# Optimization experiments

Measured on AMD Instinct MI355X. Metric: run time of the kernel, lower is better.

Reference implementation:

```python
import jax, jax.numpy as jnp
import numpy as np
from jax import lax

B, N, C, H = 8, 1024, 384, 6
D = C // H
SCALE = D ** -0.5
EPS = 1e-5


def setup_inputs() -> dict:
    key = jax.random.key(0)
    ks = jax.random.split(key, 10)
    s = 0.02
    return {
        "x": jax.random.normal(ks[0], (B, N, C), jnp.float32),
        "w_qkv": jax.random.normal(ks[1], (3 * C, C), jnp.float32) * s,
        "w_proj": jax.random.normal(ks[2], (C, C), jnp.float32) * s,
        "b_proj": jax.random.normal(ks[3], (C,), jnp.float32) * s,
        "w_kq": jax.random.normal(ks[4], (H, 1, 3, 3), jnp.float32) * 0.1,   # depthwise (groups=H)
        "b_kq": jax.random.normal(ks[5], (H,), jnp.float32) * 0.1,
        "w_head": jax.random.normal(ks[6], (H, H, 1, 1), jnp.float32) * 0.1,  # 1x1 head-mixing conv
        "b_head": jax.random.normal(ks[7], (H,), jnp.float32) * 0.1,
        "gn_w": jnp.ones((H,), jnp.float32),
        "gn_b": jnp.zeros((H,), jnp.float32),
    }


def reference(x, w_qkv, w_proj, b_proj, w_kq, b_kq, w_head, b_head, gn_w, gn_b):
    # qkv projection (torch Linear: y = x @ W.T)
    qkv = (x @ w_qkv.T).reshape(B, N, 3, H, D).transpose(2, 0, 3, 1, 4)  # [3,B,H,N,D]
    q, k, v = qkv[0], qkv[1], qkv[2]

    # attention logits [B,H,N,N]
    logits = jnp.einsum("bhnd,bhmd->bhnm", q, k) * SCALE

    # depthwise (groups=H) 3x3 conv over the NxN logit map
    logits = lax.conv_general_dilated(
        logits, w_kq, window_strides=(1, 1), padding=((1, 1), (1, 1)),
        dimension_numbers=("NCHW", "OIHW", "NCHW"), feature_group_count=H,
    ) + b_kq[None, :, None, None]

    attn = jax.nn.softmax(logits, axis=-1)

    # 1x1 conv mixing heads
    attn = jnp.einsum("oh,bhnm->bonm", w_head[:, :, 0, 0], attn) + b_head[None, :, None, None]

    # GroupNorm(num_groups=H, channels=H): per (b, head) stats over NxN
    mean = attn.mean(axis=(2, 3), keepdims=True)
    var = ((attn - mean) ** 2).mean(axis=(2, 3), keepdims=True)
    attn = (attn - mean) * lax.rsqrt(var + EPS)
    attn = attn * gn_w[None, :, None, None] + gn_b[None, :, None, None]

    out = jnp.einsum("bhnm,bhmd->bhnd", attn, v)
    out = out.transpose(0, 2, 1, 3).reshape(B, N, C)
    return out @ w_proj.T + b_proj
```

## Files before the change

### kernel.cpp

```cpp
#include <hip/hip_runtime.h>

typedef unsigned short u16;
typedef __attribute__((ext_vector_type(8))) short short8;
typedef __attribute__((ext_vector_type(4))) float f32x4;

#define MFMA(a, b, c) __builtin_amdgcn_mfma_f32_16x16x32_bf16((a), (b), (c), 0, 0, 0)

__device__ inline float bf2f(u16 u) {
  union { unsigned int i; float f; } w; w.i = ((unsigned int)u) << 16; return w.f;
}
__device__ inline u16 f2bf(float x) {
  union { float f; unsigned int i; } u; u.f = x;
  unsigned int r = u.i + 0x7fffu + ((u.i >> 16) & 1u);
  return (u16)(r >> 16);
}
__device__ inline unsigned int pk2(float a, float b) {
  return (unsigned int)f2bf(a) | ((unsigned int)f2bf(b) << 16);
}
__device__ inline void unpack8(uint4 v, float* f) {
  union { unsigned int i; float g; } c;
  c.i = v.x << 16;          f[0] = c.g;
  c.i = v.x & 0xffff0000u;  f[1] = c.g;
  c.i = v.y << 16;          f[2] = c.g;
  c.i = v.y & 0xffff0000u;  f[3] = c.g;
  c.i = v.z << 16;          f[4] = c.g;
  c.i = v.z & 0xffff0000u;  f[5] = c.g;
  c.i = v.w << 16;          f[6] = c.g;
  c.i = v.w & 0xffff0000u;  f[7] = c.g;
}

static const size_t SZ_QKV = (size_t)48 * 1024 * 64 * 2;
static const size_t SZ_MAP = (size_t)48 * 1024 * 1024 * 2;
static const size_t OFF_Q  = 0;
static const size_t OFF_K  = OFF_Q + SZ_QKV;
static const size_t OFF_VT = OFF_K + SZ_QKV;
static const size_t OFF_S  = OFF_VT + SZ_QKV;
static const size_t OFF_UG = OFF_S;
static const size_t OFF_QM = OFF_S + SZ_MAP;
static const size_t OFF_OT = OFF_QM + SZ_MAP;
static const size_t OFF_ST = OFF_OT + SZ_QKV;
static const size_t OFF_CS = OFF_ST + 896;
static const size_t OFF_AD = OFF_CS + 12288;
static const size_t OFF_AL = OFF_AD + 12288;

__global__ __launch_bounds__(256) void k_qkv(const float* __restrict__ x,
                                             const float* __restrict__ w,
                                             u16* __restrict__ qb,
                                             u16* __restrict__ kb,
                                             u16* __restrict__ vT) {
  __shared__ u16 As[128 * 64];
  __shared__ u16 Bs[128 * 64];
  const int t = threadIdx.x;
  const int m0 = blockIdx.x * 128;
  const int n0 = blockIdx.y * 128;
  const int wave = t >> 6, lane = t & 63;
  const int wm = (wave & 1) * 64, wn = (wave >> 1) * 64;
  const int fr = lane & 15;
  const int fk = (lane >> 4) * 8;
  f32x4 acc[4][4] = {};
  for (int k0 = 0; k0 < 384; k0 += 64) {
#pragma unroll
    for (int i = 0; i < 4; ++i) {
      int e = (i * 256 + t) * 8;
      int row = e >> 6, col = e & 63;
      const float* xp = &x[(size_t)(m0 + row) * 384 + k0 + col];
      const float* wp = &w[(size_t)(n0 + row) * 384 + k0 + col];
      float4 a0 = *(const float4*)xp, a1 = *(const float4*)(xp + 4);
      uint4 av; av.x = pk2(a0.x, a0.y); av.y = pk2(a0.z, a0.w);
      av.z = pk2(a1.x, a1.y); av.w = pk2(a1.z, a1.w);
      *(uint4*)&As[e] = av;
      float4 b0 = *(const float4*)wp, b1 = *(const float4*)(wp + 4);
      uint4 bv; bv.x = pk2(b0.x, b0.y); bv.y = pk2(b0.z, b0.w);
      bv.z = pk2(b1.x, b1.y); bv.w = pk2(b1.z, b1.w);
      *(uint4*)&Bs[e] = bv;
    }
    __syncthreads();
#pragma unroll
    for (int ks = 0; ks < 2; ++ks) {
      const int ko = ks * 32 + fk;
      short8 a[4], b[4];
#pragma unroll
      for (int mi = 0; mi < 4; ++mi) a[mi] = *(const short8*)&As[(wm + mi * 16 + fr) * 64 + ko];
#pragma unroll
      for (int ni = 0; ni < 4; ++ni) b[ni] = *(const short8*)&Bs[(wn + ni * 16 + fr) * 64 + ko];
#pragma unroll
      for (int mi = 0; mi < 4; ++mi)
#pragma unroll
        for (int ni = 0; ni < 4; ++ni) acc[mi][ni] = MFMA(a[mi], b[ni], acc[mi][ni]);
    }
    __syncthreads();
  }
#pragma unroll
  for (int mi = 0; mi < 4; ++mi) {
#pragma unroll
    for (int ni = 0; ni < 4; ++ni) {
      int gc = n0 + wn + ni * 16 + fr;
      int s = gc / 384;
      int rem = gc - s * 384;
      int h = rem >> 6, d = rem & 63;
#pragma unroll
      for (int r = 0; r < 4; ++r) {
        int gm = m0 + wm + mi * 16 + (lane >> 4) * 4 + r;
        int b_ = gm >> 10, n = gm & 1023;
        u16 val = f2bf(acc[mi][ni][r]);
        size_t base = (size_t)(b_ * 6 + h) << 16;
        if (s == 0)      qb[base + (size_t)n * 64 + d] = val;
        else if (s == 1) kb[base + (size_t)n * 64 + d] = val;
        else             vT[base + (size_t)d * 1024 + n] = val;
      }
    }
  }
}

__global__ __launch_bounds__(256) void k_qk(const u16* __restrict__ qb,
                                            const u16* __restrict__ kb,
                                            u16* __restrict__ S) {
  __shared__ u16 As[128 * 64];
  __shared__ u16 Bs[128 * 64];
  const int t = threadIdx.x;
  const int m0 = blockIdx.x * 128, n0 = blockIdx.y * 128;
  const int bh = blockIdx.z;
  const u16* A = qb + ((size_t)bh << 16);
  const u16* Bp = kb + ((size_t)bh << 16);
  const int wave = t >> 6, lane = t & 63;
  const int wm = (wave & 1) * 64, wn = (wave >> 1) * 64;
  const int fr = lane & 15;
  const int fk = (lane >> 4) * 8;
  f32x4 acc[4][4] = {};
#pragma unroll
  for (int i = 0; i < 4; ++i) {
    int e = (i * 256 + t) * 8;
    *(uint4*)&As[e] = *(const uint4*)&A[(size_t)m0 * 64 + e];
    *(uint4*)&Bs[e] = *(const uint4*)&Bp[(size_t)n0 * 64 + e];
  }
  __syncthreads();
#pragma unroll
  for (int ks = 0; ks < 2; ++ks) {
    const int ko = ks * 32 + fk;
    short8 a[4], b[4];
#pragma unroll
    for (int mi = 0; mi < 4; ++mi) a[mi] = *(const short8*)&As[(wm + mi * 16 + fr) * 64 + ko];
#pragma unroll
    for (int ni = 0; ni < 4; ++ni) b[ni] = *(const short8*)&Bs[(wn + ni * 16 + fr) * 64 + ko];
#pragma unroll
    for (int mi = 0; mi < 4; ++mi)
#pragma unroll
      for (int ni = 0; ni < 4; ++ni) acc[mi][ni] = MFMA(a[mi], b[ni], acc[mi][ni]);
  }
  const size_t sb = (size_t)bh << 20;
#pragma unroll
  for (int mi = 0; mi < 4; ++mi)
#pragma unroll
    for (int ni = 0; ni < 4; ++ni) {
      int gc = n0 + wn + ni * 16 + fr;
#pragma unroll
      for (int r = 0; r < 4; ++r) {
        int gm = m0 + wm + mi * 16 + (lane >> 4) * 4 + r;
        S[sb + (size_t)gm * 1024 + gc] = f2bf(acc[mi][ni][r] * 0.125f);
      }
    }
}

__global__ __launch_bounds__(256) void k_conv_softmax(const u16* __restrict__ S,
                                                      const float* __restrict__ w_kq,
                                                      u16* __restrict__ Qb) {
  __shared__ u16 Sr[10 * 1040];
  __shared__ float red[4];
  const int t = threadIdx.x;
  const int bh = blockIdx.y;
  const int h = bh % 6;
  const int r0 = blockIdx.x * 8;
  const u16* Sp = S + ((size_t)bh << 20);
  float wv[9];
#pragma unroll
  for (int i = 0; i < 9; ++i) wv[i] = w_kq[h * 9 + i];
  if (t < 10) { Sr[t * 1040 + 7] = 0; Sr[t * 1040 + 1032] = 0; }
#pragma unroll
  for (int c = 0; c < 5; ++c) {
    int e = (c * 256 + t) * 8;
    int i = e >> 10, col = e & 1023;
    int g = r0 - 1 + i;
    uint4 val = make_uint4(0u, 0u, 0u, 0u);
    if (g >= 0 && g < 1024) val = *(const uint4*)&Sp[(size_t)g * 1024 + col];
    *(uint4*)&Sr[i * 1040 + 8 + col] = val;
  }
  __syncthreads();
  const int half = t >> 7;
  const int lane = t & 63;
  const int m0 = (t & 127) * 8;
  for (int pass = 0; pass < 4; ++pass) {
    int rr = pass * 2 + half;
    float o8[8];
#pragma unroll
    for (int j = 0; j < 8; ++j) o8[j] = 0.f;
#pragma unroll
    for (int i = 0; i < 3; ++i) {
      const u16* rowp = &Sr[(rr + i) * 1040 + 8];
      float left = bf2f(rowp[m0 - 1]);
      float md[8];
      unpack8(*(const uint4*)&rowp[m0], md);
      float right = bf2f(rowp[m0 + 8]);
      float w0 = wv[i * 3 + 0], w1 = wv[i * 3 + 1], w2 = wv[i * 3 + 2];
      o8[0] += w0 * left + w1 * md[0] + w2 * md[1];
#pragma unroll
      for (int j = 1; j < 7; ++j) o8[j] += w0 * md[j - 1] + w1 * md[j] + w2 * md[j + 1];
      o8[7] += w0 * md[6] + w1 * md[7] + w2 * right;
    }
    float mx = o8[0];
#pragma unroll
    for (int j = 1; j < 8; ++j) mx = fmaxf(mx, o8[j]);
    for (int off = 32; off; off >>= 1) mx = fmaxf(mx, __shfl_xor(mx, off, 64));
    if (lane == 0) red[t >> 6] = mx;
    __syncthreads();
    float rmax = fmaxf(red[half * 2], red[half * 2 + 1]);
    __syncthreads();
    float e8[8], s = 0.f;
#pragma unroll
    for (int j = 0; j < 8; ++j) { e8[j] = __expf(o8[j] - rmax); s += e8[j]; }
    for (int off = 32; off; off >>= 1) s += __shfl_xor(s, off, 64);
    if (lane == 0) red[t >> 6] = s;
    __syncthreads();
    float rsum = red[half * 2] + red[half * 2 + 1];
    __syncthreads();
    float scale = 1024.f / rsum;
    unsigned int pk[4];
#pragma unroll
    for (int jj = 0; jj < 4; ++jj)
      pk[jj] = pk2(e8[2 * jj] * scale - 1.f, e8[2 * jj + 1] * scale - 1.f);
    int n = r0 + rr;
    *(uint4*)&Qb[((size_t)bh << 20) + (size_t)n * 1024 + m0] = make_uint4(pk[0], pk[1], pk[2], pk[3]);
  }
}

__global__ __launch_bounds__(256) void k_colsum(const u16* __restrict__ vT,
                                                float* __restrict__ colsum) {
  __shared__ float acc[64];
  const int t = threadIdx.x;
  const int bh = blockIdx.x;
  if (t < 64) acc[t] = 0.f;
  __syncthreads();
  const int lane = t & 63;
  for (int c = 0; c < 32; ++c) {
    size_t l = (size_t)c * 2048 + (size_t)t * 8;
    uint4 u = *(const uint4*)&vT[((size_t)bh << 16) + l];
    float f[8];
    unpack8(u, f);
    float part = f[0] + f[1] + f[2] + f[3] + f[4] + f[5] + f[6] + f[7];
    for (int off = 32; off; off >>= 1) part += __shfl_xor(part, off, 64);
    if (lane == 0) atomicAdd(&acc[(int)(l >> 10)], part);
  }
  __syncthreads();
  if (t < 64) colsum[bh * 64 + t] = acc[t];
}

__global__ __launch_bounds__(256) void k_pvmix(const u16* __restrict__ Qm,
                                               const u16* __restrict__ vT,
                                               const float* __restrict__ wh,
                                               float* __restrict__ Ug,
                                               float* __restrict__ stats) {
  __shared__ u16 Am[64 * 72];
  __shared__ u16 Vm[64 * 72];
  const int t = threadIdx.x;
  const int n0 = blockIdx.x * 64;
  const int bo = blockIdx.y;
  const int b_ = bo / 6, o = bo - b_ * 6;
  const int wave = t >> 6, lane = t & 63;
  const int fr = lane & 15, quad = lane >> 4;
  const int srow = t >> 3, smg8 = (t & 7) * 8;
  float wo[6];
#pragma unroll
  for (int hh = 0; hh < 6; ++hh) wo[hh] = wh[o * 6 + hh];
  const size_t qbase = ((size_t)(b_ * 6)) << 20;
  const u16* vp = vT + ((size_t)bo << 16);
  uint4 qpre[2][6];
  uint4 vpre[2];
  {
    const int m = smg8;
#pragma unroll
    for (int i = 0; i < 2; ++i)
#pragma unroll
      for (int hh = 0; hh < 6; ++hh)
        qpre[i][hh] = *(const uint4*)&Qm[qbase + (((size_t)hh) << 20) +
                                         (size_t)(n0 + i * 32 + srow) * 1024 + m];
    vpre[0] = *(const uint4*)&vp[(size_t)srow * 1024 + m];
    vpre[1] = *(const uint4*)&vp[(size_t)(32 + srow) * 1024 + m];
  }
  f32x4 acc[4] = {};
  float s1 = 0.f, s2 = 0.f;
  for (int mc = 0; mc < 16; ++mc) {
    __syncthreads();
#pragma unroll
    for (int i = 0; i < 2; ++i) {
      float mix[8] = {0.f, 0.f, 0.f, 0.f, 0.f, 0.f, 0.f, 0.f};
#pragma unroll
      for (int hh = 0; hh < 6; ++hh) {
        float qf[8];
        unpack8(qpre[i][hh], qf);
        float w = wo[hh];
#pragma unroll
        for (int j = 0; j < 8; ++j) mix[j] += w * qf[j];
      }
#pragma unroll
      for (int j = 0; j < 8; ++j) { s1 += mix[j]; s2 += mix[j] * mix[j]; }
      uint4 pk4;
      pk4.x = pk2(mix[0], mix[1]); pk4.y = pk2(mix[2], mix[3]);
      pk4.z = pk2(mix[4], mix[5]); pk4.w = pk2(mix[6], mix[7]);
      *(uint4*)&Am[(i * 32 + srow) * 72 + smg8] = pk4;
    }
    *(uint4*)&Vm[srow * 72 + smg8] = vpre[0];
    *(uint4*)&Vm[(32 + srow) * 72 + smg8] = vpre[1];
    if (mc < 15) {
      const int m = (mc + 1) * 64 + smg8;
#pragma unroll
      for (int i = 0; i < 2; ++i)
#pragma unroll
        for (int hh = 0; hh < 6; ++hh)
          qpre[i][hh] = *(const uint4*)&Qm[qbase + (((size_t)hh) << 20) +
                                           (size_t)(n0 + i * 32 + srow) * 1024 + m];
      vpre[0] = *(const uint4*)&vp[(size_t)srow * 1024 + m];
      vpre[1] = *(const uint4*)&vp[(size_t)(32 + srow) * 1024 + m];
    }
    __syncthreads();
#pragma unroll
    for (int ks = 0; ks < 2; ++ks) {
      short8 a = *(const short8*)&Am[(wave * 16 + fr) * 72 + ks * 32 + quad * 8];
#pragma unroll
      for (int ni = 0; ni < 4; ++ni) {
        short8 b = *(const short8*)&Vm[(ni * 16 + fr) * 72 + ks * 32 + quad * 8];
        acc[ni] = MFMA(a, b, acc[ni]);
      }
    }
  }
#pragma unroll
  for (int ni = 0; ni < 4; ++ni) {
    int d = ni * 16 + fr;
#pragma unroll
    for (int r = 0; r < 4; ++r) {
      int n = n0 + wave * 16 + quad * 4 + r;
      Ug[((size_t)(bo * 1024 + n)) * 64 + d] = acc[ni][r];
    }
  }
  for (int off = 32; off; off >>= 1) {
    s1 += __shfl_xor(s1, off, 64);
    s2 += __shfl_xor(s2, off, 64);
  }
  if (lane == 0) {
    atomicAdd(&stats[bo * 2 + 0], s1);
    atomicAdd(&stats[bo * 2 + 1], s2);
  }
}

__global__ __launch_bounds__(256) void k_finalize(const float* __restrict__ stats,
                                                  const float* __restrict__ colsum,
                                                  const float* __restrict__ gn_w,
                                                  const float* __restrict__ gn_b,
                                                  float* __restrict__ addend,
                                                  float* __restrict__ alphaArr) {
  int gid = blockIdx.x * 256 + threadIdx.x;
  int bo = gid >> 6, d = gid & 63;
  int o = bo % 6;
  float s1 = stats[bo * 2], s2 = stats[bo * 2 + 1];
  const float inv = 1.f / 1048576.f;
  float mu = s1 * inv;
  float var = s2 * inv - mu * mu;
  float alpha = gn_w[o] * rsqrtf(var + 1e-5f * 1048576.f);
  float beta = gn_b[o] - alpha * mu;
  addend[gid] = beta * colsum[gid];
  if (d == 0) alphaArr[bo] = alpha;
}

__global__ __launch_bounds__(256) void k_apply(const float* __restrict__ Ug,
                                               const float* __restrict__ alphaArr,
                                               const float* __restrict__ addend,
                                               u16* __restrict__ otmp) {
  int i = blockIdx.x * 256 + threadIdx.x;
  int e = i * 4;
  int d4 = e & 63;
  int n = (e >> 6) & 1023;
  int bo = e >> 16;
  float al = alphaArr[bo];
  const float* ap = &addend[bo * 64 + d4];
  float4 u = *(const float4*)&Ug[e];
  int b = bo / 6, o = bo - b * 6;
  uint2 w;
  w.x = pk2(al * u.x + ap[0], al * u.y + ap[1]);
  w.y = pk2(al * u.z + ap[2], al * u.w + ap[3]);
  *(uint2*)&otmp[((size_t)(b * 1024 + n)) * 384 + o * 64 + d4] = w;
}

__global__ __launch_bounds__(256) void k_proj(const u16* __restrict__ A,
                                              const float* __restrict__ w,
                                              const float* __restrict__ bias,
                                              float* __restrict__ out) {
  __shared__ u16 As[128 * 64];
  __shared__ u16 Bs[128 * 64];
  const int t = threadIdx.x;
  const int m0 = blockIdx.x * 128;
  const int n0 = blockIdx.y * 128;
  const int wave = t >> 6, lane = t & 63;
  const int wm = (wave & 1) * 64, wn = (wave >> 1) * 64;
  const int fr = lane & 15;
  const int fk = (lane >> 4) * 8;
  f32x4 acc[4][4] = {};
  for (int k0 = 0; k0 < 384; k0 += 64) {
#pragma unroll
    for (int i = 0; i < 4; ++i) {
      int e = (i * 256 + t) * 8;
      int row = e >> 6, col = e & 63;
      *(uint4*)&As[e] = *(const uint4*)&A[(size_t)(m0 + row) * 384 + k0 + col];
      const float* wp = &w[(size_t)(n0 + row) * 384 + k0 + col];
      float4 b0 = *(const float4*)wp, b1 = *(const float4*)(wp + 4);
      uint4 bv; bv.x = pk2(b0.x, b0.y); bv.y = pk2(b0.z, b0.w);
      bv.z = pk2(b1.x, b1.y); bv.w = pk2(b1.z, b1.w);
      *(uint4*)&Bs[e] = bv;
    }
    __syncthreads();
#pragma unroll
    for (int ks = 0; ks < 2; ++ks) {
      const int ko = ks * 32 + fk;
      short8 a[4], b[4];
#pragma unroll
      for (int mi = 0; mi < 4; ++mi) a[mi] = *(const short8*)&As[(wm + mi * 16 + fr) * 64 + ko];
#pragma unroll
      for (int ni = 0; ni < 4; ++ni) b[ni] = *(const short8*)&Bs[(wn + ni * 16 + fr) * 64 + ko];
#pragma unroll
      for (int mi = 0; mi < 4; ++mi)
#pragma unroll
        for (int ni = 0; ni < 4; ++ni) acc[mi][ni] = MFMA(a[mi], b[ni], acc[mi][ni]);
    }
    __syncthreads();
  }
#pragma unroll
  for (int mi = 0; mi < 4; ++mi)
#pragma unroll
    for (int ni = 0; ni < 4; ++ni) {
      int gc = n0 + wn + ni * 16 + fr;
      float bv = bias[gc];
#pragma unroll
      for (int r = 0; r < 4; ++r) {
        int gm = m0 + wm + mi * 16 + (lane >> 4) * 4 + r;
        out[(size_t)gm * 384 + gc] = acc[mi][ni][r] + bv;
      }
    }
}

extern "C" void kernel_launch(void* const* d_in, const int* in_sizes, int n_in,
                              void* d_out, int out_size, void* d_ws, size_t ws_size,
                              hipStream_t stream) {
  (void)in_sizes; (void)n_in; (void)out_size; (void)ws_size;
  const float* x      = (const float*)d_in[0];
  const float* w_qkv  = (const float*)d_in[1];
  const float* w_proj = (const float*)d_in[2];
  const float* b_proj = (const float*)d_in[3];
  const float* w_kq   = (const float*)d_in[4];
  const float* w_head = (const float*)d_in[6];
  const float* gn_w   = (const float*)d_in[8];
  const float* gn_b   = (const float*)d_in[9];

  char* ws = (char*)d_ws;
  u16*   qb      = (u16*)(ws + OFF_Q);
  u16*   kb      = (u16*)(ws + OFF_K);
  u16*   vT      = (u16*)(ws + OFF_VT);
  u16*   Sb      = (u16*)(ws + OFF_S);
  float* Ug      = (float*)(ws + OFF_UG);
  u16*   Qm      = (u16*)(ws + OFF_QM);
  u16*   otmp    = (u16*)(ws + OFF_OT);
  float* stats   = (float*)(ws + OFF_ST);
  float* colsum  = (float*)(ws + OFF_CS);
  float* addend  = (float*)(ws + OFF_AD);
  float* alphaA  = (float*)(ws + OFF_AL);

  hipMemsetAsync(stats, 0, 512, stream);
  k_qkv<<<dim3(64, 9), 256, 0, stream>>>(x, w_qkv, qb, kb, vT);
  k_qk<<<dim3(8, 8, 48), 256, 0, stream>>>(qb, kb, Sb);
  k_conv_softmax<<<dim3(128, 48), 256, 0, stream>>>(Sb, w_kq, Qm);
  k_colsum<<<dim3(48), 256, 0, stream>>>(vT, colsum);
  k_pvmix<<<dim3(16, 48), 256, 0, stream>>>(Qm, vT, w_head, Ug, stats);
  k_finalize<<<dim3(12), 256, 0, stream>>>(stats, colsum, gn_w, gn_b, addend, alphaA);
  k_apply<<<dim3(3072), 256, 0, stream>>>(Ug, alphaA, addend, otmp);
  k_proj<<<dim3(64, 3), 256, 0, stream>>>(otmp, w_proj, b_proj, (float*)d_out);
}
```

Before: 307.2 us.

## Fuse head-mixing into conv-softmax and split PV over key halves

```diff
diff --git a/kernel.cpp b/kernel.cpp
--- a/kernel.cpp
+++ b/kernel.cpp
@@ -43,6 +43,8 @@
 static const size_t OFF_AD = OFF_CS + 12288;
 static const size_t OFF_AL = OFF_AD + 12288;
 
+static const size_t U_ELEMS = (size_t)48 * 1024 * 64;
+
 __global__ __launch_bounds__(256) void k_qkv(const float* __restrict__ x,
                                              const float* __restrict__ w,
                                              u16* __restrict__ qb,
@@ -161,41 +163,47 @@
     }
 }
 
-__global__ __launch_bounds__(256) void k_conv_softmax(const u16* __restrict__ S,
-                                                      const float* __restrict__ w_kq,
-                                                      u16* __restrict__ Qb) {
-  __shared__ u16 Sr[10 * 1040];
-  __shared__ float red[4];
-  const int t = threadIdx.x;
-  const int bh = blockIdx.y;
-  const int h = bh % 6;
-  const int r0 = blockIdx.x * 8;
-  const u16* Sp = S + ((size_t)bh << 20);
-  float wv[9];
-#pragma unroll
-  for (int i = 0; i < 9; ++i) wv[i] = w_kq[h * 9 + i];
-  if (t < 10) { Sr[t * 1040 + 7] = 0; Sr[t * 1040 + 1032] = 0; }
-#pragma unroll
-  for (int c = 0; c < 5; ++c) {
-    int e = (c * 256 + t) * 8;
-    int i = e >> 10, col = e & 1023;
-    int g = r0 - 1 + i;
+__global__ __launch_bounds__(256) void k_conv_softmax_mix(const u16* __restrict__ S,
+                                                          const float* __restrict__ w_kq,
+                                                          const float* __restrict__ wh,
+                                                          u16* __restrict__ Qb) {
+  __shared__ u16 Sr[24 * 1040];
+  __shared__ float redA[4], redB[4];
+  const int t = threadIdx.x;
+  const int b = blockIdx.y;
+  const int n0 = blockIdx.x * 2;
+  if (t < 24) { Sr[t * 1040 + 7] = 0; Sr[t * 1040 + 1032] = 0; }
+#pragma unroll
+  for (int c = 0; c < 12; ++c) {
+    int lid = c * 256 + t;
+    int hrow = lid >> 7;
+    int col8 = (lid & 127) * 8;
+    int h = hrow >> 2, i = hrow & 3;
+    int g = n0 - 1 + i;
     uint4 val = make_uint4(0u, 0u, 0u, 0u);
-    if (g >= 0 && g < 1024) val = *(const uint4*)&Sp[(size_t)g * 1024 + col];
-    *(uint4*)&Sr[i * 1040 + 8 + col] = val;
+    if (g >= 0 && g < 1024)
+      val = *(const uint4*)&S[(((size_t)(b * 6 + h)) << 20) + (size_t)g * 1024 + col8];
+    *(uint4*)&Sr[hrow * 1040 + 8 + col8] = val;
   }
   __syncthreads();
-  const int half = t >> 7;
+  const int row = t >> 7;
+  const int wave = t >> 6;
   const int lane = t & 63;
   const int m0 = (t & 127) * 8;
-  for (int pass = 0; pass < 4; ++pass) {
-    int rr = pass * 2 + half;
-    float o8[8];
-#pragma unroll
-    for (int j = 0; j < 8; ++j) o8[j] = 0.f;
+  const int n = n0 + row;
+  float mix[6][8];
+#pragma unroll
+  for (int o = 0; o < 6; ++o)
+#pragma unroll
+    for (int j = 0; j < 8; ++j) mix[o][j] = 0.f;
+  for (int h = 0; h < 6; ++h) {
+    float wv[9];
+#pragma unroll
+    for (int i = 0; i < 9; ++i) wv[i] = w_kq[h * 9 + i];
+    float o8[8] = {0.f, 0.f, 0.f, 0.f, 0.f, 0.f, 0.f, 0.f};
 #pragma unroll
     for (int i = 0; i < 3; ++i) {
-      const u16* rowp = &Sr[(rr + i) * 1040 + 8];
+      const u16* rowp = &Sr[(h * 4 + row + i) * 1040 + 8];
       float left = bf2f(rowp[m0 - 1]);
       float md[8];
       unpack8(*(const uint4*)&rowp[m0], md);
@@ -210,25 +218,34 @@
 #pragma unroll
     for (int j = 1; j < 8; ++j) mx = fmaxf(mx, o8[j]);
     for (int off = 32; off; off >>= 1) mx = fmaxf(mx, __shfl_xor(mx, off, 64));
-    if (lane == 0) red[t >> 6] = mx;
-    __syncthreads();
-    float rmax = fmaxf(red[half * 2], red[half * 2 + 1]);
-    __syncthreads();
+    if (lane == 0) redA[wave] = mx;
+    __syncthreads();
+    float rmax = fmaxf(redA[row * 2], redA[row * 2 + 1]);
     float e8[8], s = 0.f;
 #pragma unroll
     for (int j = 0; j < 8; ++j) { e8[j] = __expf(o8[j] - rmax); s += e8[j]; }
     for (int off = 32; off; off >>= 1) s += __shfl_xor(s, off, 64);
-    if (lane == 0) red[t >> 6] = s;
-    __syncthreads();
-    float rsum = red[half * 2] + red[half * 2 + 1];
-    __syncthreads();
+    if (lane == 0) redB[wave] = s;
+    __syncthreads();
+    float rsum = redB[row * 2] + redB[row * 2 + 1];
     float scale = 1024.f / rsum;
-    unsigned int pk[4];
-#pragma unroll
-    for (int jj = 0; jj < 4; ++jj)
-      pk[jj] = pk2(e8[2 * jj] * scale - 1.f, e8[2 * jj + 1] * scale - 1.f);
-    int n = r0 + rr;
-    *(uint4*)&Qb[((size_t)bh << 20) + (size_t)n * 1024 + m0] = make_uint4(pk[0], pk[1], pk[2], pk[3]);
+    const float w0h = wh[0 * 6 + h], w1h = wh[1 * 6 + h], w2h = wh[2 * 6 + h],
+                w3h = wh[3 * 6 + h], w4h = wh[4 * 6 + h], w5h = wh[5 * 6 + h];
+#pragma unroll
+    for (int j = 0; j < 8; ++j) {
+      float p = e8[j] * scale - 1.f;
+      mix[0][j] += w0h * p; mix[1][j] += w1h * p; mix[2][j] += w2h * p;
+      mix[3][j] += w3h * p; mix[4][j] += w4h * p; mix[5][j] += w5h * p;
+    }
+  }
+#pragma unroll
+  for (int o = 0; o < 6; ++o) {
+    uint4 pk4;
+    pk4.x = pk2(mix[o][0], mix[o][1]);
+    pk4.y = pk2(mix[o][2], mix[o][3]);
+    pk4.z = pk2(mix[o][4], mix[o][5]);
+    pk4.w = pk2(mix[o][6], mix[o][7]);
+    *(uint4*)&Qb[(((size_t)(b * 6 + o)) << 20) + (size_t)n * 1024 + m0] = pk4;
   }
 }
 
@@ -253,70 +270,51 @@
   if (t < 64) colsum[bh * 64 + t] = acc[t];
 }
 
-__global__ __launch_bounds__(256) void k_pvmix(const u16* __restrict__ Qm,
-                                               const u16* __restrict__ vT,
-                                               const float* __restrict__ wh,
-                                               float* __restrict__ Ug,
-                                               float* __restrict__ stats) {
+__global__ __launch_bounds__(256) void k_pv(const u16* __restrict__ Qm,
+                                            const u16* __restrict__ vT,
+                                            float* __restrict__ Ug,
+                                            float* __restrict__ stats) {
   __shared__ u16 Am[64 * 72];
   __shared__ u16 Vm[64 * 72];
   const int t = threadIdx.x;
   const int n0 = blockIdx.x * 64;
   const int bo = blockIdx.y;
-  const int b_ = bo / 6, o = bo - b_ * 6;
+  const int z = blockIdx.z;
   const int wave = t >> 6, lane = t & 63;
   const int fr = lane & 15, quad = lane >> 4;
   const int srow = t >> 3, smg8 = (t & 7) * 8;
-  float wo[6];
-#pragma unroll
-  for (int hh = 0; hh < 6; ++hh) wo[hh] = wh[o * 6 + hh];
-  const size_t qbase = ((size_t)(b_ * 6)) << 20;
+  const u16* qp = Qm + ((size_t)bo << 20);
   const u16* vp = vT + ((size_t)bo << 16);
-  uint4 qpre[2][6];
-  uint4 vpre[2];
+  const int mbase = z * 512;
+  uint4 qpre[2], vpre[2];
   {
-    const int m = smg8;
-#pragma unroll
-    for (int i = 0; i < 2; ++i)
-#pragma unroll
-      for (int hh = 0; hh < 6; ++hh)
-        qpre[i][hh] = *(const uint4*)&Qm[qbase + (((size_t)hh) << 20) +
-                                         (size_t)(n0 + i * 32 + srow) * 1024 + m];
+    const int m = mbase + smg8;
+    qpre[0] = *(const uint4*)&qp[(size_t)(n0 + srow) * 1024 + m];
+    qpre[1] = *(const uint4*)&qp[(size_t)(n0 + 32 + srow) * 1024 + m];
     vpre[0] = *(const uint4*)&vp[(size_t)srow * 1024 + m];
     vpre[1] = *(const uint4*)&vp[(size_t)(32 + srow) * 1024 + m];
   }
   f32x4 acc[4] = {};
   float s1 = 0.f, s2 = 0.f;
-  for (int mc = 0; mc < 16; ++mc) {
-    __syncthreads();
-#pragma unroll
-    for (int i = 0; i < 2; ++i) {
-      float mix[8] = {0.f, 0.f, 0.f, 0.f, 0.f, 0.f, 0.f, 0.f};
-#pragma unroll
-      for (int hh = 0; hh < 6; ++hh) {
-        float qf[8];
-        unpack8(qpre[i][hh], qf);
-        float w = wo[hh];
-#pragma unroll
-        for (int j = 0; j < 8; ++j) mix[j] += w * qf[j];
-      }
-#pragma unroll
-      for (int j = 0; j < 8; ++j) { s1 += mix[j]; s2 += mix[j] * mix[j]; }
-      uint4 pk4;
-      pk4.x = pk2(mix[0], mix[1]); pk4.y = pk2(mix[2], mix[3]);
-      pk4.z = pk2(mix[4], mix[5]); pk4.w = pk2(mix[6], mix[7]);
-      *(uint4*)&Am[(i * 32 + srow) * 72 + smg8] = pk4;
-    }
+  for (int mc = 0; mc < 8; ++mc) {
+    __syncthreads();
+    *(uint4*)&Am[srow * 72 + smg8] = qpre[0];
+    *(uint4*)&Am[(32 + srow) * 72 + smg8] = qpre[1];
     *(uint4*)&Vm[srow * 72 + smg8] = vpre[0];
     *(uint4*)&Vm[(32 + srow) * 72 + smg8] = vpre[1];
-    if (mc < 15) {
-      const int m = (mc + 1) * 64 + smg8;
-#pragma unroll
-      for (int i = 0; i < 2; ++i)
-#pragma unroll
-        for (int hh = 0; hh < 6; ++hh)
-          qpre[i][hh] = *(const uint4*)&Qm[qbase + (((size_t)hh) << 20) +
-                                           (size_t)(n0 + i * 32 + srow) * 1024 + m];
+    {
+      float f[8];
+      unpack8(qpre[0], f);
+#pragma unroll
+      for (int j = 0; j < 8; ++j) { s1 += f[j]; s2 += f[j] * f[j]; }
+      unpack8(qpre[1], f);
+#pragma unroll
+      for (int j = 0; j < 8; ++j) { s1 += f[j]; s2 += f[j] * f[j]; }
+    }
+    if (mc < 7) {
+      const int m = mbase + (mc + 1) * 64 + smg8;
+      qpre[0] = *(const uint4*)&qp[(size_t)(n0 + srow) * 1024 + m];
+      qpre[1] = *(const uint4*)&qp[(size_t)(n0 + 32 + srow) * 1024 + m];
       vpre[0] = *(const uint4*)&vp[(size_t)srow * 1024 + m];
       vpre[1] = *(const uint4*)&vp[(size_t)(32 + srow) * 1024 + m];
     }
@@ -331,13 +329,14 @@
       }
     }
   }
+  float* Up = Ug + (size_t)z * U_ELEMS;
 #pragma unroll
   for (int ni = 0; ni < 4; ++ni) {
     int d = ni * 16 + fr;
 #pragma unroll
     for (int r = 0; r < 4; ++r) {
       int n = n0 + wave * 16 + quad * 4 + r;
-      Ug[((size_t)(bo * 1024 + n)) * 64 + d] = acc[ni][r];
+      Up[((size_t)(bo * 1024 + n)) * 64 + d] = acc[ni][r];
     }
   }
   for (int off = 32; off; off >>= 1) {
@@ -380,11 +379,13 @@
   int bo = e >> 16;
   float al = alphaArr[bo];
   const float* ap = &addend[bo * 64 + d4];
-  float4 u = *(const float4*)&Ug[e];
+  float4 u0 = *(const float4*)&Ug[e];
+  float4 u1 = *(const float4*)&Ug[U_ELEMS + e];
+  float ux = u0.x + u1.x, uy = u0.y + u1.y, uz = u0.z + u1.z, uw = u0.w + u1.w;
   int b = bo / 6, o = bo - b * 6;
   uint2 w;
-  w.x = pk2(al * u.x + ap[0], al * u.y + ap[1]);
-  w.y = pk2(al * u.z + ap[2], al * u.w + ap[3]);
+  w.x = pk2(al * ux + ap[0], al * uy + ap[1]);
+  w.y = pk2(al * uz + ap[2], al * uw + ap[3]);
   *(uint2*)&otmp[((size_t)(b * 1024 + n)) * 384 + o * 64 + d4] = w;
 }
 
@@ -473,9 +474,9 @@
   hipMemsetAsync(stats, 0, 512, stream);
   k_qkv<<<dim3(64, 9), 256, 0, stream>>>(x, w_qkv, qb, kb, vT);
   k_qk<<<dim3(8, 8, 48), 256, 0, stream>>>(qb, kb, Sb);
-  k_conv_softmax<<<dim3(128, 48), 256, 0, stream>>>(Sb, w_kq, Qm);
+  k_conv_softmax_mix<<<dim3(512, 8), 256, 0, stream>>>(Sb, w_kq, w_head, Qm);
   k_colsum<<<dim3(48), 256, 0, stream>>>(vT, colsum);
-  k_pvmix<<<dim3(16, 48), 256, 0, stream>>>(Qm, vT, w_head, Ug, stats);
+  k_pv<<<dim3(16, 48, 2), 256, 0, stream>>>(Qm, vT, Ug, stats);
   k_finalize<<<dim3(12), 256, 0, stream>>>(stats, colsum, gn_w, gn_b, addend, alphaA);
   k_apply<<<dim3(3072), 256, 0, stream>>>(Ug, alphaA, addend, otmp);
   k_proj<<<dim3(64, 3), 256, 0, stream>>>(otmp, w_proj, b_proj, (float*)d_out);
```

After: 345.9 us. 12.6% more time.

## Stage GEMM epilogues through LDS for coalesced stores and fuse colsum into QKV

Applied to the files above, without the earlier changes.

```diff
diff --git a/kernel.cpp b/kernel.cpp
--- a/kernel.cpp
+++ b/kernel.cpp
@@ -43,13 +43,15 @@
 static const size_t OFF_AD = OFF_CS + 12288;
 static const size_t OFF_AL = OFF_AD + 12288;
 
-__global__ __launch_bounds__(256) void k_qkv(const float* __restrict__ x,
-                                             const float* __restrict__ w,
-                                             u16* __restrict__ qb,
-                                             u16* __restrict__ kb,
-                                             u16* __restrict__ vT) {
-  __shared__ u16 As[128 * 64];
-  __shared__ u16 Bs[128 * 64];
+__global__ __launch_bounds__(256, 3) void k_qkv(const float* __restrict__ x,
+                                                const float* __restrict__ w,
+                                                u16* __restrict__ qb,
+                                                u16* __restrict__ kb,
+                                                u16* __restrict__ vT,
+                                                float* __restrict__ colsum) {
+  __shared__ u16 SH[16384];
+  u16* As = SH;
+  u16* Bs = SH + 8192;
   const int t = threadIdx.x;
   const int m0 = blockIdx.x * 128;
   const int n0 = blockIdx.y * 128;
@@ -90,33 +92,58 @@
     }
     __syncthreads();
   }
-#pragma unroll
-  for (int mi = 0; mi < 4; ++mi) {
+  u16* st = &SH[wave * 4096];
+  const int gcb = n0 + wn;
+  const int s = gcb / 384;
+  const int remb = gcb - s * 384;
+  const int h = remb >> 6;
+#pragma unroll
+  for (int mi = 0; mi < 4; ++mi)
+#pragma unroll
+    for (int ni = 0; ni < 4; ++ni)
+#pragma unroll
+      for (int r = 0; r < 4; ++r) {
+        int rl = mi * 16 + (lane >> 4) * 4 + r;
+        int cl = ni * 16 + fr;
+        u16 val = f2bf(acc[mi][ni][r]);
+        if (s == 2) st[cl * 64 + rl] = val;
+        else        st[rl * 64 + cl] = val;
+      }
+  const int gm0 = m0 + wm;
+  const int b_ = gm0 >> 10;
+  const size_t base = (size_t)(b_ * 6 + h) << 16;
+  const int nloc = gm0 & 1023;
+  const int r8 = lane >> 3, c8 = (lane & 7) * 8;
+#pragma unroll
+  for (int i = 0; i < 8; ++i) {
+    int lrow = i * 8 + r8;
+    uint4 v = *(const uint4*)&st[lrow * 64 + c8];
+    if (s == 0)      *(uint4*)&qb[base + (size_t)(nloc + lrow) * 64 + c8] = v;
+    else if (s == 1) *(uint4*)&kb[base + (size_t)(nloc + lrow) * 64 + c8] = v;
+    else             *(uint4*)&vT[base + (size_t)lrow * 1024 + nloc + c8] = v;
+  }
+  if (s == 2) {
 #pragma unroll
     for (int ni = 0; ni < 4; ++ni) {
-      int gc = n0 + wn + ni * 16 + fr;
-      int s = gc / 384;
-      int rem = gc - s * 384;
-      int h = rem >> 6, d = rem & 63;
-#pragma unroll
-      for (int r = 0; r < 4; ++r) {
-        int gm = m0 + wm + mi * 16 + (lane >> 4) * 4 + r;
-        int b_ = gm >> 10, n = gm & 1023;
-        u16 val = f2bf(acc[mi][ni][r]);
-        size_t base = (size_t)(b_ * 6 + h) << 16;
-        if (s == 0)      qb[base + (size_t)n * 64 + d] = val;
-        else if (s == 1) kb[base + (size_t)n * 64 + d] = val;
-        else             vT[base + (size_t)d * 1024 + n] = val;
-      }
-    }
-  }
-}
-
-__global__ __launch_bounds__(256) void k_qk(const u16* __restrict__ qb,
-                                            const u16* __restrict__ kb,
-                                            u16* __restrict__ S) {
-  __shared__ u16 As[128 * 64];
-  __shared__ u16 Bs[128 * 64];
+      float p = 0.f;
+#pragma unroll
+      for (int mi = 0; mi < 4; ++mi)
+#pragma unroll
+        for (int r = 0; r < 4; ++r) p += bf2f(f2bf(acc[mi][ni][r]));
+      p += __shfl_xor(p, 16, 64);
+      p += __shfl_xor(p, 32, 64);
+      if ((lane >> 4) == 0)
+        atomicAdd(&colsum[(b_ * 6 + h) * 64 + ni * 16 + fr], p);
+    }
+  }
+}
+
+__global__ __launch_bounds__(256, 3) void k_qk(const u16* __restrict__ qb,
+                                               const u16* __restrict__ kb,
+                                               u16* __restrict__ S) {
+  __shared__ u16 SH[16384];
+  u16* As = SH;
+  u16* Bs = SH + 8192;
   const int t = threadIdx.x;
   const int m0 = blockIdx.x * 128, n0 = blockIdx.y * 128;
   const int bh = blockIdx.z;
@@ -147,18 +174,24 @@
 #pragma unroll
       for (int ni = 0; ni < 4; ++ni) acc[mi][ni] = MFMA(a[mi], b[ni], acc[mi][ni]);
   }
+  __syncthreads();
+  u16* st = &SH[wave * 4096];
+#pragma unroll
+  for (int mi = 0; mi < 4; ++mi)
+#pragma unroll
+    for (int ni = 0; ni < 4; ++ni)
+#pragma unroll
+      for (int r = 0; r < 4; ++r)
+        st[(mi * 16 + (lane >> 4) * 4 + r) * 64 + ni * 16 + fr] = f2bf(acc[mi][ni][r] * 0.125f);
   const size_t sb = (size_t)bh << 20;
-#pragma unroll
-  for (int mi = 0; mi < 4; ++mi)
-#pragma unroll
-    for (int ni = 0; ni < 4; ++ni) {
-      int gc = n0 + wn + ni * 16 + fr;
-#pragma unroll
-      for (int r = 0; r < 4; ++r) {
-        int gm = m0 + wm + mi * 16 + (lane >> 4) * 4 + r;
-        S[sb + (size_t)gm * 1024 + gc] = f2bf(acc[mi][ni][r] * 0.125f);
-      }
-    }
+  const int grow0 = m0 + wm, gcol0 = n0 + wn;
+  const int r8 = lane >> 3, c8 = (lane & 7) * 8;
+#pragma unroll
+  for (int i = 0; i < 8; ++i) {
+    int lrow = i * 8 + r8;
+    uint4 v = *(const uint4*)&st[lrow * 64 + c8];
+    *(uint4*)&S[sb + (size_t)(grow0 + lrow) * 1024 + gcol0 + c8] = v;
+  }
 }
 
 __global__ __launch_bounds__(256) void k_conv_softmax(const u16* __restrict__ S,
@@ -232,34 +265,14 @@
   }
 }
 
-__global__ __launch_bounds__(256) void k_colsum(const u16* __restrict__ vT,
-                                                float* __restrict__ colsum) {
-  __shared__ float acc[64];
-  const int t = threadIdx.x;
-  const int bh = blockIdx.x;
-  if (t < 64) acc[t] = 0.f;
-  __syncthreads();
-  const int lane = t & 63;
-  for (int c = 0; c < 32; ++c) {
-    size_t l = (size_t)c * 2048 + (size_t)t * 8;
-    uint4 u = *(const uint4*)&vT[((size_t)bh << 16) + l];
-    float f[8];
-    unpack8(u, f);
-    float part = f[0] + f[1] + f[2] + f[3] + f[4] + f[5] + f[6] + f[7];
-    for (int off = 32; off; off >>= 1) part += __shfl_xor(part, off, 64);
-    if (lane == 0) atomicAdd(&acc[(int)(l >> 10)], part);
-  }
-  __syncthreads();
-  if (t < 64) colsum[bh * 64 + t] = acc[t];
-}
-
 __global__ __launch_bounds__(256) void k_pvmix(const u16* __restrict__ Qm,
                                                const u16* __restrict__ vT,
                                                const float* __restrict__ wh,
                                                float* __restrict__ Ug,
                                                float* __restrict__ stats) {
-  __shared__ u16 Am[64 * 72];
-  __shared__ u16 Vm[64 * 72];
+  __shared__ u16 SH[2 * 64 * 72];
+  u16* Am = SH;
+  u16* Vm = SH + 64 * 72;
   const int t = threadIdx.x;
   const int n0 = blockIdx.x * 64;
   const int bo = blockIdx.y;
@@ -331,14 +344,19 @@
       }
     }
   }
-#pragma unroll
-  for (int ni = 0; ni < 4; ++ni) {
-    int d = ni * 16 + fr;
-#pragma unroll
-    for (int r = 0; r < 4; ++r) {
-      int n = n0 + wave * 16 + quad * 4 + r;
-      Ug[((size_t)(bo * 1024 + n)) * 64 + d] = acc[ni][r];
-    }
+  __syncthreads();
+  float* FS = (float*)SH;
+#pragma unroll
+  for (int ni = 0; ni < 4; ++ni)
+#pragma unroll
+    for (int r = 0; r < 4; ++r)
+      FS[(wave * 16 + quad * 4 + r) * 64 + ni * 16 + fr] = acc[ni][r];
+  __syncthreads();
+  float* Up = Ug + ((size_t)(bo * 1024 + n0)) * 64;
+#pragma unroll
+  for (int j = 0; j < 4; ++j) {
+    int oo = j * 1024 + t * 4;
+    *(float4*)&Up[oo] = *(const float4*)&FS[oo];
   }
   for (int off = 32; off; off >>= 1) {
     s1 += __shfl_xor(s1, off, 64);
@@ -388,12 +406,13 @@
   *(uint2*)&otmp[((size_t)(b * 1024 + n)) * 384 + o * 64 + d4] = w;
 }
 
-__global__ __launch_bounds__(256) void k_proj(const u16* __restrict__ A,
-                                              const float* __restrict__ w,
-                                              const float* __restrict__ bias,
-                                              float* __restrict__ out) {
-  __shared__ u16 As[128 * 64];
-  __shared__ u16 Bs[128 * 64];
+__global__ __launch_bounds__(256, 3) void k_proj(const u16* __restrict__ A,
+                                                 const float* __restrict__ w,
+                                                 const float* __restrict__ bias,
+                                                 float* __restrict__ out) {
+  __shared__ u16 SH[16384];
+  u16* As = SH;
+  u16* Bs = SH + 8192;
   const int t = threadIdx.x;
   const int m0 = blockIdx.x * 128;
   const int n0 = blockIdx.y * 128;
@@ -430,18 +449,32 @@
     }
     __syncthreads();
   }
-#pragma unroll
-  for (int mi = 0; mi < 4; ++mi)
-#pragma unroll
-    for (int ni = 0; ni < 4; ++ni) {
-      int gc = n0 + wn + ni * 16 + fr;
-      float bv = bias[gc];
-#pragma unroll
-      for (int r = 0; r < 4; ++r) {
-        int gm = m0 + wm + mi * 16 + (lane >> 4) * 4 + r;
-        out[(size_t)gm * 384 + gc] = acc[mi][ni][r] + bv;
+  float* FS = (float*)SH;
+  float* fst = &FS[wave * 2048];
+  float bv[4];
+#pragma unroll
+  for (int ni = 0; ni < 4; ++ni) bv[ni] = bias[n0 + wn + ni * 16 + fr];
+#pragma unroll
+  for (int half = 0; half < 2; ++half) {
+#pragma unroll
+    for (int mi2 = 0; mi2 < 2; ++mi2) {
+      int mi = half * 2 + mi2;
+#pragma unroll
+      for (int ni = 0; ni < 4; ++ni)
+#pragma unroll
+        for (int r = 0; r < 4; ++r)
+          fst[(mi2 * 16 + (lane >> 4) * 4 + r) * 64 + ni * 16 + fr] = acc[mi][ni][r] + bv[ni];
+    }
+#pragma unroll
+    for (int g = 0; g < 4; ++g)
+#pragma unroll
+      for (int i2 = 0; i2 < 2; ++i2) {
+        int lrow = g * 8 + (lane >> 3);
+        int colf = i2 * 32 + (lane & 7) * 4;
+        float4 v = *(const float4*)&fst[lrow * 64 + colf];
+        *(float4*)&out[(size_t)(m0 + wm + half * 32 + lrow) * 384 + n0 + wn + colf] = v;
       }
-    }
+  }
 }
 
 extern "C" void kernel_launch(void* const* d_in, const int* in_sizes, int n_in,
@@ -470,11 +503,10 @@
   float* addend  = (float*)(ws + OFF_AD);
   float* alphaA  = (float*)(ws + OFF_AL);
 
-  hipMemsetAsync(stats, 0, 512, stream);
-  k_qkv<<<dim3(64, 9), 256, 0, stream>>>(x, w_qkv, qb, kb, vT);
+  hipMemsetAsync(stats, 0, 896 + 12288, stream);
+  k_qkv<<<dim3(64, 9), 256, 0, stream>>>(x, w_qkv, qb, kb, vT, colsum);
   k_qk<<<dim3(8, 8, 48), 256, 0, stream>>>(qb, kb, Sb);
   k_conv_softmax<<<dim3(128, 48), 256, 0, stream>>>(Sb, w_kq, Qm);
-  k_colsum<<<dim3(48), 256, 0, stream>>>(vT, colsum);
   k_pvmix<<<dim3(16, 48), 256, 0, stream>>>(Qm, vT, w_head, Ug, stats);
   k_finalize<<<dim3(12), 256, 0, stream>>>(stats, colsum, gn_w, gn_b, addend, alphaA);
   k_apply<<<dim3(3072), 256, 0, stream>>>(Ug, alphaA, addend, otmp);
```

New measurement: 286.5 us. -6.7%, faster.
